# Performance work log

Hardware: AMD Instinct MI355X
Metric: run time of the kernel (lower is better)

Reference implementation:

```python
import jax, jax.numpy as jnp
import numpy as np

B, C, N = 8, 256, 2048
H = max(1, C // 8)  # hidden = in_channels // 8 = 32


def setup_inputs() -> dict:
    key = jax.random.key(0)
    ks = jax.random.split(key, 7)
    s = 0.05
    return {
        "x": jax.random.normal(ks[0], (B, C, N), dtype=jnp.float32),
        "wq": jax.random.normal(ks[1], (H, C), dtype=jnp.float32) * s,
        "bq": jax.random.normal(ks[2], (H,), dtype=jnp.float32) * s,
        "wk": jax.random.normal(ks[3], (H, C), dtype=jnp.float32) * s,
        "bk": jax.random.normal(ks[4], (H,), dtype=jnp.float32) * s,
        "wv": jax.random.normal(ks[5], (C, C), dtype=jnp.float32) * s,
        "bv": jax.random.normal(ks[6], (C,), dtype=jnp.float32) * s,
    }


def reference(x, wq, bq, wk, bk, wv, bv):
    # 1x1 Conv1d == per-position linear: weight [out, in]
    q = jnp.einsum('bcn,hc->bnh', x, wq) + bq                  # [B, N, H] (already permuted)
    k = jnp.einsum('bcn,hc->bhn', x, wk) + bk[None, :, None]   # [B, H, N]
    v = jnp.einsum('bcn,dc->bdn', x, wv) + bv[None, :, None]   # [B, C, N]
    energy = jnp.einsum('bnh,bhm->bnm', q, k)                  # [B, N, N] (no scaling, as in source)
    weights = jax.nn.softmax(energy, axis=-1)                  # softmax over last dim
    # out = bmm(value, weights^T): out[b,c,i] = sum_j v[b,c,j] * weights[b,i,j]
    out = jnp.einsum('bcj,bij->bci', v, weights)               # [B, C, N]
    return out + x
```

## Files before the change

### kernel.cpp

```cpp
#include <hip/hip_runtime.h>
#include <hip/hip_bf16.h>
#include <cstdint>
#include <cstddef>

#define B_ 8
#define C_ 256
#define N_ 2048
#define H_ 32

typedef __bf16 bf8 __attribute__((ext_vector_type(8)));
typedef float f4 __attribute__((ext_vector_type(4)));
typedef float f16v __attribute__((ext_vector_type(16)));

__device__ inline void gload_lds16(const void* g, void* l) {
  __builtin_amdgcn_global_load_lds(
      (const __attribute__((address_space(1))) unsigned int*)g,
      (__attribute__((address_space(3))) unsigned int*)l, 16, 0, 0);
}

__global__ __launch_bounds__(256) void pack_kernel(
    const float* __restrict__ wq, const float* __restrict__ wk,
    const float* __restrict__ wv, const float* __restrict__ bq,
    const float* __restrict__ bk, const float* __restrict__ bv,
    __hip_bfloat16* __restrict__ wpk, float* __restrict__ bpk) {
  int r = blockIdx.x, c = threadIdx.x;
  float v;
  if (r < 256)      v = wv[r * 256 + c];
  else if (r < 288) v = wq[(r - 256) * 256 + c];
  else              v = wk[(r - 288) * 256 + c];
  wpk[r * 256 + c] = __float2bfloat16(v);
  if (c == 0) bpk[r] = (r < 256) ? bv[r] : (r < 288 ? bq[r - 256] : bk[r - 288]);
}

__global__ __launch_bounds__(256) void proj_kernel(
    const float* __restrict__ x, const __hip_bfloat16* __restrict__ wpk,
    const float* __restrict__ bpk, __hip_bfloat16* __restrict__ vbf,
    __hip_bfloat16* __restrict__ qkb) {
  __shared__ __attribute__((aligned(16))) __hip_bfloat16 As[2][320 * 32];
  int tid = threadIdx.x, wv = tid >> 6, lane = tid & 63;
  int b = blockIdx.y;
  int n0 = blockIdx.x * 32;
  int fcol = lane & 15, hi4 = lane >> 4;
  int grow = lane >> 2, gc = (lane & 3) * 8;
  const float* xb = x + (size_t)b * C_ * N_;

#pragma unroll
  for (int g = 0; g < 5; ++g)
    gload_lds16(wpk + (size_t)(wv * 80 + g * 16 + grow) * 256 + gc,
                &As[0][(wv * 80 + g * 16) * 32]);
  float xr[2][8];
#pragma unroll
  for (int j = 0; j < 2; ++j)
#pragma unroll
    for (int e = 0; e < 8; ++e)
      xr[j][e] = xb[(size_t)(hi4 * 8 + e) * N_ + n0 + j * 16 + fcol];

  f4 acc[5][2] = {};
  for (int t = 0; t < 8; ++t) {
    int buf = t & 1;
    __syncthreads();
    if (t < 7) {
      int k1 = (t + 1) * 32;
#pragma unroll
      for (int g = 0; g < 5; ++g)
        gload_lds16(wpk + (size_t)(wv * 80 + g * 16 + grow) * 256 + k1 + gc,
                    &As[buf ^ 1][(wv * 80 + g * 16) * 32]);
    }
    bf8 bfr[2];
#pragma unroll
    for (int j = 0; j < 2; ++j)
#pragma unroll
      for (int e = 0; e < 8; ++e) bfr[j][e] = (__bf16)xr[j][e];
    if (t < 7) {
      int k1 = (t + 1) * 32;
#pragma unroll
      for (int j = 0; j < 2; ++j)
#pragma unroll
        for (int e = 0; e < 8; ++e)
          xr[j][e] = xb[(size_t)(k1 + hi4 * 8 + e) * N_ + n0 + j * 16 + fcol];
    }
#pragma unroll
    for (int s = 0; s < 5; ++s) {
      bf8 af = *(const bf8*)&As[buf][(wv * 80 + s * 16 + fcol) * 32 + hi4 * 8];
      acc[s][0] = __builtin_amdgcn_mfma_f32_16x16x32_bf16(af, bfr[0], acc[s][0], 0, 0, 0);
      acc[s][1] = __builtin_amdgcn_mfma_f32_16x16x32_bf16(af, bfr[1], acc[s][1], 0, 0, 0);
    }
  }
  int rq = hi4 * 4;
#pragma unroll
  for (int s = 0; s < 5; ++s)
#pragma unroll
    for (int r = 0; r < 4; ++r) {
      int m = wv * 80 + s * 16 + rq + r;
      float bias = bpk[m];
#pragma unroll
      for (int j = 0; j < 2; ++j) {
        int n = n0 + j * 16 + fcol;
        float val = acc[s][j][r] + bias;
        if (m < 256)
          vbf[((size_t)b * C_ + m) * N_ + n] = __float2bfloat16(val);
        else
          qkb[((size_t)b * N_ + n) * 64 + (m - 256)] = __float2bfloat16(val);
      }
    }
}

#define FJT 64

__global__ __launch_bounds__(256, 2) void fused_attn(
    const __hip_bfloat16* __restrict__ qk,
    const __hip_bfloat16* __restrict__ vbf,
    const float* __restrict__ x, float* __restrict__ out) {
  __shared__ __attribute__((aligned(16))) __hip_bfloat16 vS[2][128 * FJT];
  __shared__ __attribute__((aligned(16))) __hip_bfloat16 pS[2][2][32 * 72];
  __shared__ float lSp[2][2][32];
  int tid = threadIdx.x;
  int wv = tid >> 6, lane = tid & 63;
  int iw = wv >> 1, cw = wv & 1;
  int blk = blockIdx.x;
  int b = blk & 7;
  int rest = blk >> 3;
  int c0 = (rest & 1) * 128;
  int i0 = (rest >> 1) * 64;
  int l31 = lane & 31, hi = lane >> 5;

  const __hip_bfloat16* qkB = qk + (size_t)b * N_ * 64;
  bf8 qf0 = *(const bf8*)&qkB[(size_t)(i0 + iw * 32 + l31) * 64 + hi * 8];
  bf8 qf1 = *(const bf8*)&qkB[(size_t)(i0 + iw * 32 + l31) * 64 + 16 + hi * 8];

  const __hip_bfloat16* vB = vbf + ((size_t)b * C_ + c0) * N_;
  int grow = lane >> 3;
  int gch = ((lane & 7) ^ (grow & 7)) * 8;
  int kjrow = cw * 32 + l31;

  bf8 kf0, kf1, kn0, kn1;
#pragma unroll
  for (int g = 0; g < 4; ++g)
    gload_lds16(vB + (size_t)(wv * 32 + g * 8 + grow) * N_ + gch,
                &vS[0][(wv * 32 + g * 8) * FJT]);
  kf0 = *(const bf8*)&qkB[(size_t)kjrow * 64 + 32 + hi * 8];
  kf1 = *(const bf8*)&qkB[(size_t)kjrow * 64 + 32 + 16 + hi * 8];

  f16v acc0 = {}, acc1 = {};
  float lp[16];
#pragma unroll
  for (int r = 0; r < 16; ++r) lp[r] = 0.f;

  for (int t = 0; t < N_ / FJT; ++t) {
    int buf = t & 1;
    f16v s = {};
    s = __builtin_amdgcn_mfma_f32_32x32x16_bf16(qf0, kf0, s, 0, 0, 0);
    s = __builtin_amdgcn_mfma_f32_32x32x16_bf16(qf1, kf1, s, 0, 0, 0);
    __hip_bfloat16* pW = &pS[buf][iw][0];
#pragma unroll
    for (int r = 0; r < 16; ++r) {
      float p = __expf(s[r]);
      lp[r] += p;
      int row = (r & 3) + 8 * (r >> 2) + 4 * hi;
      pW[row * 72 + cw * 32 + l31] = __float2bfloat16(p);
    }
    __syncthreads();
    if (t + 1 < N_ / FJT) {
      int j1 = (t + 1) * FJT;
#pragma unroll
      for (int g = 0; g < 4; ++g)
        gload_lds16(vB + (size_t)(wv * 32 + g * 8 + grow) * N_ + j1 + gch,
                    &vS[buf ^ 1][(wv * 32 + g * 8) * FJT]);
      kn0 = *(const bf8*)&qkB[(size_t)(j1 + kjrow) * 64 + 32 + hi * 8];
      kn1 = *(const bf8*)&qkB[(size_t)(j1 + kjrow) * 64 + 32 + 16 + hi * 8];
    }
    const __hip_bfloat16* pR = &pS[buf][iw][0];
    int r0 = cw * 64 + l31, r1 = r0 + 32;
    int sw = r0 & 7;
#pragma unroll
    for (int jc = 0; jc < 4; ++jc) {
      int ch = jc * 2 + hi;
      bf8 pf = *(const bf8*)&pR[l31 * 72 + jc * 16 + hi * 8];
      bf8 vf0 = *(const bf8*)&vS[buf][r0 * FJT + ((ch ^ sw) * 8)];
      bf8 vf1 = *(const bf8*)&vS[buf][r1 * FJT + ((ch ^ sw) * 8)];
      acc0 = __builtin_amdgcn_mfma_f32_32x32x16_bf16(vf0, pf, acc0, 0, 0, 0);
      acc1 = __builtin_amdgcn_mfma_f32_32x32x16_bf16(vf1, pf, acc1, 0, 0, 0);
    }
    if (t + 1 < N_ / FJT) { kf0 = kn0; kf1 = kn1; }
  }

#pragma unroll
  for (int r = 0; r < 16; ++r) {
    float v = lp[r];
    v += __shfl_xor(v, 1); v += __shfl_xor(v, 2); v += __shfl_xor(v, 4);
    v += __shfl_xor(v, 8); v += __shfl_xor(v, 16);
    lp[r] = v;
  }
  if (l31 == 0) {
#pragma unroll
    for (int r = 0; r < 16; ++r)
      lSp[iw][cw][(r & 3) + 8 * (r >> 2) + 4 * hi] = lp[r];
  }
  __syncthreads();
  float linv = 1.0f / (lSp[iw][0][l31] + lSp[iw][1][l31]);
  int i = i0 + iw * 32 + l31;
  const float* xr = x + (size_t)b * C_ * N_;
  float* op = out + (size_t)b * C_ * N_;
#pragma unroll
  for (int r = 0; r < 16; ++r) {
    int row = (r & 3) + 8 * (r >> 2) + 4 * hi;
    size_t o0 = (size_t)(c0 + cw * 64 + row) * N_ + i;
    op[o0] = acc0[r] * linv + xr[o0];
    size_t o1 = o0 + (size_t)32 * N_;
    op[o1] = acc1[r] * linv + xr[o1];
  }
}

extern "C" void kernel_launch(void* const* d_in, const int* in_sizes, int n_in,
                              void* d_out, int out_size, void* d_ws, size_t ws_size,
                              hipStream_t stream) {
  const float* x  = (const float*)d_in[0];
  const float* wq = (const float*)d_in[1];
  const float* bq = (const float*)d_in[2];
  const float* wk = (const float*)d_in[3];
  const float* bk = (const float*)d_in[4];
  const float* wv = (const float*)d_in[5];
  const float* bv = (const float*)d_in[6];
  float* out = (float*)d_out;

  char* ws = (char*)d_ws;
  __hip_bfloat16* qkb = (__hip_bfloat16*)ws;
  __hip_bfloat16* vbf = (__hip_bfloat16*)(ws + (2u << 20));
  __hip_bfloat16* wpk = (__hip_bfloat16*)(ws + (10u << 20));
  float*          bpk = (float*)(ws + (10u << 20) + (256u << 10));

  pack_kernel<<<dim3(320), 256, 0, stream>>>(wq, wk, wv, bq, bk, bv, wpk, bpk);
  proj_kernel<<<dim3(N_ / 32, B_), 256, 0, stream>>>(x, wpk, bpk, vbf, qkb);
  fused_attn<<<dim3(512), 256, 0, stream>>>(qkb, vbf, x, out);
}
```

Before: 136.0 us.

## Load V fragments directly to registers and remap waves in fused attention

Reworks the fused attention kernel so each wave owns 32 channel rows and loads its V operands straight from global memory into registers, prefetched one tile ahead, instead of staging V through LDS. The score MFMA is transposed so P is written to a shared 64x88 tile as packed bf16x4 stores, and each wave reads P for both 32-row i halves. V rows are padded to a stride of 2064 to avoid cache-set conflicts, and the barrier is replaced by an explicit lgkmcnt wait plus s_barrier with raised priority around the PV MFMAs. This removes the LDS traffic and swizzle for V, but depends on global-load latency being hidden by the register prefetch and increases register pressure.

New measurement: 127.5 us. -6.3%, faster.

```diff
diff --git a/kernel.cpp b/kernel.cpp
--- a/kernel.cpp
+++ b/kernel.cpp
@@ -7,8 +7,11 @@
 #define C_ 256
 #define N_ 2048
 #define H_ 32
+#define VP_ 2064
+#define NT_ (N_ / 64)
 
 typedef __bf16 bf8 __attribute__((ext_vector_type(8)));
+typedef __bf16 bf4 __attribute__((ext_vector_type(4)));
 typedef float f4 __attribute__((ext_vector_type(4)));
 typedef float f16v __attribute__((ext_vector_type(16)));
 
@@ -98,116 +101,116 @@
         int n = n0 + j * 16 + fcol;
         float val = acc[s][j][r] + bias;
         if (m < 256)
-          vbf[((size_t)b * C_ + m) * N_ + n] = __float2bfloat16(val);
+          vbf[((size_t)b * C_ + m) * VP_ + n] = __float2bfloat16(val);
         else
           qkb[((size_t)b * N_ + n) * 64 + (m - 256)] = __float2bfloat16(val);
       }
     }
 }
-
-#define FJT 64
 
 __global__ __launch_bounds__(256, 2) void fused_attn(
     const __hip_bfloat16* __restrict__ qk,
     const __hip_bfloat16* __restrict__ vbf,
     const float* __restrict__ x, float* __restrict__ out) {
-  __shared__ __attribute__((aligned(16))) __hip_bfloat16 vS[2][128 * FJT];
-  __shared__ __attribute__((aligned(16))) __hip_bfloat16 pS[2][2][32 * 72];
-  __shared__ float lSp[2][2][32];
+  __shared__ __attribute__((aligned(16))) __hip_bfloat16 pS[2][64][88];
+  __shared__ float lSp[2][64];
   int tid = threadIdx.x;
   int wv = tid >> 6, lane = tid & 63;
-  int iw = wv >> 1, cw = wv & 1;
+  int l31 = lane & 31, hi = lane >> 5;
+  int ws_i = wv >> 1, ws_j = wv & 1;
   int blk = blockIdx.x;
   int b = blk & 7;
   int rest = blk >> 3;
   int c0 = (rest & 1) * 128;
   int i0 = (rest >> 1) * 64;
-  int l31 = lane & 31, hi = lane >> 5;
 
   const __hip_bfloat16* qkB = qk + (size_t)b * N_ * 64;
-  bf8 qf0 = *(const bf8*)&qkB[(size_t)(i0 + iw * 32 + l31) * 64 + hi * 8];
-  bf8 qf1 = *(const bf8*)&qkB[(size_t)(i0 + iw * 32 + l31) * 64 + 16 + hi * 8];
-
-  const __hip_bfloat16* vB = vbf + ((size_t)b * C_ + c0) * N_;
-  int grow = lane >> 3;
-  int gch = ((lane & 7) ^ (grow & 7)) * 8;
-  int kjrow = cw * 32 + l31;
-
-  bf8 kf0, kf1, kn0, kn1;
-#pragma unroll
-  for (int g = 0; g < 4; ++g)
-    gload_lds16(vB + (size_t)(wv * 32 + g * 8 + grow) * N_ + gch,
-                &vS[0][(wv * 32 + g * 8) * FJT]);
-  kf0 = *(const bf8*)&qkB[(size_t)kjrow * 64 + 32 + hi * 8];
-  kf1 = *(const bf8*)&qkB[(size_t)kjrow * 64 + 32 + 16 + hi * 8];
+  const __hip_bfloat16* qp = qkB + (size_t)(i0 + ws_i * 32 + l31) * 64 + hi * 8;
+  bf8 qf0 = *(const bf8*)qp;
+  bf8 qf1 = *(const bf8*)(qp + 16);
+  const __hip_bfloat16* kp = qkB + (size_t)(ws_j * 32 + l31) * 64 + 32 + hi * 8;
+  bf8 kf0 = *(const bf8*)kp;
+  bf8 kf1 = *(const bf8*)(kp + 16);
+  const __hip_bfloat16* vR =
+      vbf + ((size_t)b * C_ + c0 + wv * 32 + l31) * VP_ + hi * 8;
+  bf8 vf0 = *(const bf8*)vR;
+  bf8 vf1 = *(const bf8*)(vR + 16);
+  bf8 vf2 = *(const bf8*)(vR + 32);
+  bf8 vf3 = *(const bf8*)(vR + 48);
 
   f16v acc0 = {}, acc1 = {};
-  float lp[16];
-#pragma unroll
-  for (int r = 0; r < 16; ++r) lp[r] = 0.f;
-
-  for (int t = 0; t < N_ / FJT; ++t) {
+  float lp0 = 0.f, lp1 = 0.f;
+
+#define PV_STEP(KB, VA)                                                       \
+  {                                                                           \
+    const __hip_bfloat16* pr = &pS[buf][l31][(KB) * 16 + hi * 8];             \
+    bf8 pf0 = *(const bf8*)pr;                                                \
+    bf8 pf1 = *(const bf8*)(pr + 32 * 88);                                    \
+    acc0 = __builtin_amdgcn_mfma_f32_32x32x16_bf16(VA, pf0, acc0, 0, 0, 0);   \
+    acc1 = __builtin_amdgcn_mfma_f32_32x32x16_bf16(VA, pf1, acc1, 0, 0, 0);   \
+  }
+
+  for (int t = 0; t < NT_; ++t) {
     int buf = t & 1;
     f16v s = {};
-    s = __builtin_amdgcn_mfma_f32_32x32x16_bf16(qf0, kf0, s, 0, 0, 0);
-    s = __builtin_amdgcn_mfma_f32_32x32x16_bf16(qf1, kf1, s, 0, 0, 0);
-    __hip_bfloat16* pW = &pS[buf][iw][0];
-#pragma unroll
-    for (int r = 0; r < 16; ++r) {
-      float p = __expf(s[r]);
-      lp[r] += p;
-      int row = (r & 3) + 8 * (r >> 2) + 4 * hi;
-      pW[row * 72 + cw * 32 + l31] = __float2bfloat16(p);
-    }
-    __syncthreads();
-    if (t + 1 < N_ / FJT) {
-      int j1 = (t + 1) * FJT;
-#pragma unroll
-      for (int g = 0; g < 4; ++g)
-        gload_lds16(vB + (size_t)(wv * 32 + g * 8 + grow) * N_ + j1 + gch,
-                    &vS[buf ^ 1][(wv * 32 + g * 8) * FJT]);
-      kn0 = *(const bf8*)&qkB[(size_t)(j1 + kjrow) * 64 + 32 + hi * 8];
-      kn1 = *(const bf8*)&qkB[(size_t)(j1 + kjrow) * 64 + 32 + 16 + hi * 8];
-    }
-    const __hip_bfloat16* pR = &pS[buf][iw][0];
-    int r0 = cw * 64 + l31, r1 = r0 + 32;
-    int sw = r0 & 7;
-#pragma unroll
-    for (int jc = 0; jc < 4; ++jc) {
-      int ch = jc * 2 + hi;
-      bf8 pf = *(const bf8*)&pR[l31 * 72 + jc * 16 + hi * 8];
-      bf8 vf0 = *(const bf8*)&vS[buf][r0 * FJT + ((ch ^ sw) * 8)];
-      bf8 vf1 = *(const bf8*)&vS[buf][r1 * FJT + ((ch ^ sw) * 8)];
-      acc0 = __builtin_amdgcn_mfma_f32_32x32x16_bf16(vf0, pf, acc0, 0, 0, 0);
-      acc1 = __builtin_amdgcn_mfma_f32_32x32x16_bf16(vf1, pf, acc1, 0, 0, 0);
-    }
-    if (t + 1 < N_ / FJT) { kf0 = kn0; kf1 = kn1; }
-  }
-
-#pragma unroll
-  for (int r = 0; r < 16; ++r) {
-    float v = lp[r];
-    v += __shfl_xor(v, 1); v += __shfl_xor(v, 2); v += __shfl_xor(v, 4);
-    v += __shfl_xor(v, 8); v += __shfl_xor(v, 16);
-    lp[r] = v;
-  }
-  if (l31 == 0) {
-#pragma unroll
-    for (int r = 0; r < 16; ++r)
-      lSp[iw][cw][(r & 3) + 8 * (r >> 2) + 4 * hi] = lp[r];
-  }
+    s = __builtin_amdgcn_mfma_f32_32x32x16_bf16(kf0, qf0, s, 0, 0, 0);
+    s = __builtin_amdgcn_mfma_f32_32x32x16_bf16(kf1, qf1, s, 0, 0, 0);
+    bf8 kn0, kn1, vn0, vn1, vn2, vn3;
+    if (t + 1 < NT_) {
+      const __hip_bfloat16* kpn = kp + (size_t)(t + 1) * 64 * 64;
+      kn0 = *(const bf8*)kpn;
+      kn1 = *(const bf8*)(kpn + 16);
+      const __hip_bfloat16* vpn = vR + (t + 1) * 64;
+      vn0 = *(const bf8*)vpn;
+      vn1 = *(const bf8*)(vpn + 16);
+      vn2 = *(const bf8*)(vpn + 32);
+      vn3 = *(const bf8*)(vpn + 48);
+    }
+#pragma unroll
+    for (int r = 0; r < 16; ++r) s[r] = __expf(s[r]);
+#pragma unroll
+    for (int r = 0; r < 16; r += 2) { lp0 += s[r]; lp1 += s[r + 1]; }
+    __hip_bfloat16* pw = &pS[buf][ws_i * 32 + l31][ws_j * 32 + 4 * hi];
+#pragma unroll
+    for (int q = 0; q < 4; ++q) {
+      bf4 tb;
+      tb[0] = (__bf16)s[4 * q + 0];
+      tb[1] = (__bf16)s[4 * q + 1];
+      tb[2] = (__bf16)s[4 * q + 2];
+      tb[3] = (__bf16)s[4 * q + 3];
+      *(bf4*)(pw + 8 * q) = tb;
+    }
+    asm volatile("s_waitcnt lgkmcnt(0)" ::: "memory");
+    __builtin_amdgcn_s_barrier();
+    asm volatile("" ::: "memory");
+    __builtin_amdgcn_s_setprio(1);
+    PV_STEP(0, vf0)
+    PV_STEP(1, vf1)
+    PV_STEP(2, vf2)
+    PV_STEP(3, vf3)
+    __builtin_amdgcn_s_setprio(0);
+    if (t + 1 < NT_) {
+      kf0 = kn0; kf1 = kn1;
+      vf0 = vn0; vf1 = vn1; vf2 = vn2; vf3 = vn3;
+    }
+  }
+#undef PV_STEP
+
+  float lp = lp0 + lp1;
+  lp += __shfl_xor(lp, 32);
+  if (lane < 32) lSp[ws_j][ws_i * 32 + l31] = lp;
   __syncthreads();
-  float linv = 1.0f / (lSp[iw][0][l31] + lSp[iw][1][l31]);
-  int i = i0 + iw * 32 + l31;
+  float linv0 = 1.0f / (lSp[0][l31] + lSp[1][l31]);
+  float linv1 = 1.0f / (lSp[0][32 + l31] + lSp[1][32 + l31]);
+
   const float* xr = x + (size_t)b * C_ * N_;
   float* op = out + (size_t)b * C_ * N_;
 #pragma unroll
   for (int r = 0; r < 16; ++r) {
-    int row = (r & 3) + 8 * (r >> 2) + 4 * hi;
-    size_t o0 = (size_t)(c0 + cw * 64 + row) * N_ + i;
-    op[o0] = acc0[r] * linv + xr[o0];
-    size_t o1 = o0 + (size_t)32 * N_;
-    op[o1] = acc1[r] * linv + xr[o1];
+    int crow = (r & 3) + 8 * (r >> 2) + 4 * hi;
+    size_t o = (size_t)(c0 + wv * 32 + crow) * N_ + i0 + l31;
+    op[o] = acc0[r] * linv0 + xr[o];
+    op[o + 32] = acc1[r] * linv1 + xr[o + 32];
   }
 }
 
@@ -226,8 +229,8 @@
   char* ws = (char*)d_ws;
   __hip_bfloat16* qkb = (__hip_bfloat16*)ws;
   __hip_bfloat16* vbf = (__hip_bfloat16*)(ws + (2u << 20));
-  __hip_bfloat16* wpk = (__hip_bfloat16*)(ws + (10u << 20));
-  float*          bpk = (float*)(ws + (10u << 20) + (256u << 10));
+  __hip_bfloat16* wpk = (__hip_bfloat16*)(ws + 10551296u);
+  float*          bpk = (float*)(ws + 10551296u + 163840u);
 
   pack_kernel<<<dim3(320), 256, 0, stream>>>(wq, wk, wv, bq, bk, bv, wpk, bpk);
   proj_kernel<<<dim3(N_ / 32, B_), 256, 0, stream>>>(x, wpk, bpk, vbf, qkb);
```
